# Kernel tuning notes

Hardware: AMD Instinct MI355X
Metric: run time of the kernel (lower is better)

Reference implementation:

```python
import jax, jax.numpy as jnp
import numpy as np

N = 1_000_000
VOCAB = 50_000
EMBED_DIM = 128
ENCODE_DIM = 128


def _random_preorder_tree(n, seed=0):
    """Generate a random tree whose nodes are numbered in pre-order DFS.
    Returns subtree_end[i] = index of the last node in node i's subtree (inclusive)."""
    rng = np.random.default_rng(seed)
    parent = np.empty(n, dtype=np.int64)
    parent[0] = -1
    stack = [0]
    pops = rng.geometric(0.5, size=n) - 1  # how far up to climb before attaching
    for i in range(1, n):
        npop = min(int(pops[i]), len(stack) - 1)
        for _ in range(npop):
            stack.pop()
        parent[i] = stack[-1]
        stack.append(i)
    end = np.arange(n, dtype=np.int64)
    for i in range(n - 1, 0, -1):
        p = parent[i]
        if end[p] < end[i]:
            end[p] = end[i]
    return end


def setup_inputs() -> dict:
    key = jax.random.key(0)
    k1, k2, k3, k4 = jax.random.split(key, 4)
    tokens = jax.random.randint(k1, (N,), 0, VOCAB, dtype=jnp.int64).astype(jnp.int32)
    subtree_end = jnp.asarray(_random_preorder_tree(N), dtype=jnp.int32)
    embedding_weight = jax.random.normal(k2, (VOCAB, EMBED_DIM), dtype=jnp.float32)
    W = jax.random.normal(k3, (ENCODE_DIM, EMBED_DIM), dtype=jnp.float32) * (1.0 / np.sqrt(EMBED_DIM))
    b = jax.random.normal(k4, (ENCODE_DIM,), dtype=jnp.float32) * 0.01
    return {"tokens": tokens, "subtree_end": subtree_end,
            "embedding_weight": embedding_weight, "W": W, "b": b}


def reference(tokens, subtree_end, embedding_weight, W, b):
    # Per-node contribution: x_i = Linear(Embed(token_i))          [N, encode_dim]
    x = embedding_weight[tokens] @ W.T + b
    # h_i = sum of x over subtree(i). With pre-order DFS numbering, the subtree
    # of i is the contiguous range [i, subtree_end[i]], so use an inclusive
    # prefix sum: h_i = S[end_i] - S[i] + x_i.
    S = jnp.cumsum(x, axis=0)                                      # [N, encode_dim]
    h = S[subtree_end] - S + x                                     # [N, encode_dim]
    # pool = max over all node hidden states (order-independent)
    return jnp.max(h, axis=0)                                      # [encode_dim]
```

## Files before the change

kernel.cpp:

```cpp
#include <hip/hip_runtime.h>
#include <hip/hip_bf16.h>

#define D      128
#define LG     8
#define CHUNK  256

typedef __attribute__((ext_vector_type(8))) short          short8;
typedef __attribute__((ext_vector_type(8))) unsigned short ushort8;
typedef __attribute__((ext_vector_type(4))) float          floatx4;

__device__ inline float b2f(unsigned short u) {
    return __uint_as_float(((unsigned)u) << 16);
}
__device__ inline short f2bf(float f) {
    __hip_bfloat16 h = __float2bfloat16(f);
    unsigned short u;
    __builtin_memcpy(&u, &h, 2);
    return (short)u;
}

__global__ void init_out_kernel(float* out, int out_size) {
    int t = threadIdx.x;
    if (t < out_size) out[t] = -INFINITY;
}

__global__ void local_scan_kernel(const int* __restrict__ tokens,
                                  const float* __restrict__ emb,
                                  unsigned short* __restrict__ S,
                                  float* __restrict__ sumE, int n) {
    __shared__ int toks[CHUNK];
    int c  = blockIdx.x;
    int i0 = c << LG;
    int cnt = min(CHUNK, n - i0);
    for (int t = threadIdx.x; t < cnt; t += 128) toks[t] = tokens[i0 + t];
    __syncthreads();
    int d = threadIdx.x;
    float run = 0.f;
    #pragma unroll 8
    for (int j = 0; j < cnt; ++j) {
        run += emb[(size_t)toks[j] * D + d];
        S[(size_t)(i0 + j) * D + d] = (unsigned short)f2bf(run);
    }
    sumE[(size_t)c * D + d] = run;
}

__global__ void scan_kernel(float* sumE, int C) {
    int d    = blockIdx.x;
    int lane = threadIdx.x;
    float carry = 0.f;
    for (int c0 = 0; c0 < C; c0 += 64) {
        int c = c0 + lane;
        float v = (c < C) ? sumE[(size_t)c * D + d] : 0.f;
        float incl = v;
        #pragma unroll
        for (int off = 1; off < 64; off <<= 1) {
            float t = __shfl_up(incl, off);
            if (lane >= off) incl += t;
        }
        if (c < C) sumE[(size_t)c * D + d] = carry + incl - v;
        carry += __shfl(incl, 63);
    }
}

__device__ inline void atomicMaxF(float* addr, float v) {
    if (v >= 0.f) atomicMax((int*)addr, __float_as_int(v));
    else          atomicMin((unsigned int*)addr, __float_as_uint(v));
}

__global__ __launch_bounds__(256, 2) void max_pass_kernel(
        const int* __restrict__ ends, const unsigned short* __restrict__ S,
        const float* __restrict__ prefE, const float* __restrict__ W,
        const float* __restrict__ bvec, float* __restrict__ out, int n) {
    __shared__ ushort8 Sl[257 * 16];
    __shared__ int   s_end[CHUNK];
    __shared__ float red[4][4][16];
    int tid = threadIdx.x;
    int cb  = blockIdx.x;
    int i0  = cb << LG;
    int cnt = min(CHUNK, n - i0);

    for (int t = tid; t < CHUNK; t += 256)
        s_end[t] = (i0 + t < n) ? ends[i0 + t] : (i0 + t);
    const ushort8* gsrc = (const ushort8*)(S + (size_t)i0 * D);
    int units = cnt * 16;
    for (int u = tid; u < units; u += 256) {
        int r = u >> 4, q = u & 15;
        Sl[(r << 4) | (q ^ (r & 7))] = gsrc[u];
    }
    ushort8 z = {0, 0, 0, 0, 0, 0, 0, 0};
    for (int u = units + tid; u < 257 * 16; u += 256) {
        int r = u >> 4, q = u & 15;
        Sl[(r << 4) | (q ^ (r & 7))] = z;
    }

    int lane = tid & 63, wid = tid >> 6;
    int c  = lane & 15;
    int kg = lane >> 4;
    int tw   = wid & 1;
    int pair = wid >> 1;

    short8 Wf[4][4];
    float  bc[4];
    #pragma unroll
    for (int tl = 0; tl < 4; ++tl) {
        int tg = tw * 4 + tl;
        const float* wr = W + (size_t)(tg * 16 + c) * D + kg * 8;
        bc[tl] = bvec[tg * 16 + c];
        #pragma unroll
        for (int kk = 0; kk < 4; ++kk) {
            floatx4 f0 = *(const floatx4*)(wr + kk * 32);
            floatx4 f1 = *(const floatx4*)(wr + kk * 32 + 4);
            short8 w;
            #pragma unroll
            for (int j = 0; j < 4; ++j) { w[j] = f2bf(f0[j]); w[j + 4] = f2bf(f1[j]); }
            Wf[tl][kk] = w;
        }
    }
    float mx[4];
    #pragma unroll
    for (int tl = 0; tl < 4; ++tl) mx[tl] = -INFINITY;

    __syncthreads();

    int tiles = (cnt + 15) >> 4;
    int Tend  = min(pair * 8 + 8, tiles);
    for (int T = pair * 8; T < Tend; ++T) {
        int j    = (T << 4) + c;
        int node = i0 + j;
        bool vr  = node < n;
        int e    = s_end[j];
        int eloc = e - i0;
        bool cross = vr && (eloc >= CHUNK);
        int re = cross ? j : eloc;
        int rp = (j == 0) ? 256 : (j - 1);

        short8 Ae[4], Ap[4];
        #pragma unroll
        for (int kk = 0; kk < 4; ++kk) {
            ushort8 ve = Sl[(re << 4) | ((kk * 4 + kg) ^ (re & 7))];
            ushort8 vp = Sl[(rp << 4) | ((kk * 4 + kg) ^ (rp & 7))];
            __builtin_memcpy(&Ae[kk], &ve, 16);
            __builtin_memcpy(&Ap[kk], &vp, 16);
        }
        if (cross) {
            int ce = e >> LG;
            const ushort8* ge = (const ushort8*)(S + (size_t)e * D);
            const float* qe = prefE + (size_t)ce * D + kg * 8;
            const float* qc = prefE + (size_t)cb * D + kg * 8;
            #pragma unroll
            for (int kk = 0; kk < 4; ++kk) {
                ushort8 se = ge[kk * 4 + kg];
                floatx4 qe0 = *(const floatx4*)(qe + kk * 32);
                floatx4 qe1 = *(const floatx4*)(qe + kk * 32 + 4);
                floatx4 qc0 = *(const floatx4*)(qc + kk * 32);
                floatx4 qc1 = *(const floatx4*)(qc + kk * 32 + 4);
                short8 a;
                #pragma unroll
                for (int jj = 0; jj < 4; ++jj) {
                    a[jj]     = f2bf(b2f(se[jj])     + qe0[jj] - qc0[jj]);
                    a[jj + 4] = f2bf(b2f(se[jj + 4]) + qe1[jj] - qc1[jj]);
                }
                Ae[kk] = a;
            }
        }
        floatx4 cnt4;
        #pragma unroll
        for (int i = 0; i < 4; ++i) {
            int nd = i0 + (T << 4) + kg * 4 + i;
            float ee = (float)__shfl(e, kg * 4 + i);
            cnt4[i] = (nd < n) ? (ee - (float)nd + 1.f) : 0.f;
        }
        #pragma unroll
        for (int tl = 0; tl < 4; ++tl) {
            floatx4 ae = {0.f, 0.f, 0.f, 0.f};
            floatx4 ap = {0.f, 0.f, 0.f, 0.f};
            ae = __builtin_amdgcn_mfma_f32_16x16x32_bf16(Ae[0], Wf[tl][0], ae, 0, 0, 0);
            ae = __builtin_amdgcn_mfma_f32_16x16x32_bf16(Ae[1], Wf[tl][1], ae, 0, 0, 0);
            ae = __builtin_amdgcn_mfma_f32_16x16x32_bf16(Ae[2], Wf[tl][2], ae, 0, 0, 0);
            ae = __builtin_amdgcn_mfma_f32_16x16x32_bf16(Ae[3], Wf[tl][3], ae, 0, 0, 0);
            ap = __builtin_amdgcn_mfma_f32_16x16x32_bf16(Ap[0], Wf[tl][0], ap, 0, 0, 0);
            ap = __builtin_amdgcn_mfma_f32_16x16x32_bf16(Ap[1], Wf[tl][1], ap, 0, 0, 0);
            ap = __builtin_amdgcn_mfma_f32_16x16x32_bf16(Ap[2], Wf[tl][2], ap, 0, 0, 0);
            ap = __builtin_amdgcn_mfma_f32_16x16x32_bf16(Ap[3], Wf[tl][3], ap, 0, 0, 0);
            #pragma unroll
            for (int i = 0; i < 4; ++i) {
                int nd = i0 + (T << 4) + kg * 4 + i;
                float h = (ae[i] - ap[i]) + cnt4[i] * bc[tl];
                if (nd < n) mx[tl] = fmaxf(mx[tl], h);
            }
        }
    }
    #pragma unroll
    for (int tl = 0; tl < 4; ++tl) {
        float v = mx[tl];
        v = fmaxf(v, __shfl_xor(v, 16));
        v = fmaxf(v, __shfl_xor(v, 32));
        mx[tl] = v;
    }
    if (kg == 0) {
        #pragma unroll
        for (int tl = 0; tl < 4; ++tl) red[wid][tl][c] = mx[tl];
    }
    __syncthreads();
    if (tid < 128) {
        int twf = tid >> 6;
        int tl  = (tid >> 4) & 3;
        int cc  = tid & 15;
        float v = fmaxf(red[twf][tl][cc], red[twf + 2][tl][cc]);
        atomicMaxF(&out[(twf * 4 + tl) * 16 + cc], v);
    }
}

extern "C" void kernel_launch(void* const* d_in, const int* in_sizes, int n_in,
                              void* d_out, int out_size, void* d_ws, size_t ws_size,
                              hipStream_t stream) {
    const int*   tokens = (const int*)d_in[0];
    const int*   ends   = (const int*)d_in[1];
    const float* emb    = (const float*)d_in[2];
    const float* W      = (const float*)d_in[3];
    const float* bvec   = (const float*)d_in[4];
    float* out = (float*)d_out;
    int n = in_sizes[0];
    int C = (n + CHUNK - 1) >> LG;

    unsigned short* S    = (unsigned short*)d_ws;
    float*          sumE = (float*)(S + (size_t)n * D);

    init_out_kernel<<<1, 128, 0, stream>>>(out, out_size);
    local_scan_kernel<<<C, 128, 0, stream>>>(tokens, emb, S, sumE, n);
    scan_kernel<<<128, 64, 0, stream>>>(sumE, C);
    max_pass_kernel<<<C, 256, 0, stream>>>(ends, S, sumE, W, bvec, out, n);
}
```

Measured before the change: 331.1 us.

## Fuse projection into local scan and handle in-chunk subtrees before global scan

Applies the linear projection per node with MFMA inside the first kernel, then scans the projected values in shared memory and stores the bf16 chunk-local prefix. In-chunk subtrees are max-reduced in that same kernel, so the second pass only processes nodes whose subtree crosses a chunk boundary, found by ballot. This removes the full re-read of S and the second round of MFMAs over every node. The cost is a serial 256-step shared-memory scan done by only half the threads, and irregular per-node gathers in the cross kernel.

```diff
diff --git a/kernel.cpp b/kernel.cpp
--- a/kernel.cpp
+++ b/kernel.cpp
@@ -8,15 +8,22 @@
 typedef __attribute__((ext_vector_type(8))) short          short8;
 typedef __attribute__((ext_vector_type(8))) unsigned short ushort8;
 typedef __attribute__((ext_vector_type(4))) float          floatx4;
+typedef __attribute__((ext_vector_type(2))) float          floatx2;
+typedef __attribute__((ext_vector_type(2))) unsigned       uintx2;
 
 __device__ inline float b2f(unsigned short u) {
     return __uint_as_float(((unsigned)u) << 16);
 }
-__device__ inline short f2bf(float f) {
+__device__ inline unsigned short f2bf(float f) {
     __hip_bfloat16 h = __float2bfloat16(f);
     unsigned short u;
     __builtin_memcpy(&u, &h, 2);
-    return (short)u;
+    return u;
+}
+
+__device__ inline void atomicMaxF(float* addr, float v) {
+    if (v >= 0.f) atomicMax((int*)addr, __float_as_int(v));
+    else          atomicMin((unsigned int*)addr, __float_as_uint(v));
 }
 
 __global__ void init_out_kernel(float* out, int out_size) {
@@ -24,24 +31,127 @@
     if (t < out_size) out[t] = -INFINITY;
 }
 
-__global__ void local_scan_kernel(const int* __restrict__ tokens,
-                                  const float* __restrict__ emb,
-                                  unsigned short* __restrict__ S,
-                                  float* __restrict__ sumE, int n) {
-    __shared__ int toks[CHUNK];
-    int c  = blockIdx.x;
-    int i0 = c << LG;
-    int cnt = min(CHUNK, n - i0);
-    for (int t = threadIdx.x; t < cnt; t += 128) toks[t] = tokens[i0 + t];
-    __syncthreads();
-    int d = threadIdx.x;
-    float run = 0.f;
-    #pragma unroll 8
-    for (int j = 0; j < cnt; ++j) {
-        run += emb[(size_t)toks[j] * D + d];
-        S[(size_t)(i0 + j) * D + d] = (unsigned short)f2bf(run);
-    }
-    sumE[(size_t)c * D + d] = run;
+__global__ __launch_bounds__(256, 2) void fused_kernel(
+        const int* __restrict__ tokens, const int* __restrict__ ends,
+        const float* __restrict__ emb, const float* __restrict__ W,
+        const float* __restrict__ bvec, unsigned short* __restrict__ T_sp,
+        float* __restrict__ sumE, float* __restrict__ out, int n) {
+    __shared__ ushort8 Tl[CHUNK * 16];
+    __shared__ int s_tok[CHUNK];
+    __shared__ int s_end[CHUNK];
+    __shared__ floatx2 redf[4][64];
+    int tid = threadIdx.x, cb = blockIdx.x;
+    int i0 = cb << LG, cnt = min(CHUNK, n - i0);
+    {
+        int gi = i0 + tid;
+        s_tok[tid] = tokens[min(gi, n - 1)];
+        s_end[tid] = (gi < n) ? ends[gi] : gi;
+    }
+    __syncthreads();
+
+    int lane = tid & 63, wid = tid >> 6;
+    int c = lane & 15, kg = lane >> 4;
+    int tw = wid & 1, pair = wid >> 1;
+
+    short8 Wf[4][4];
+    #pragma unroll
+    for (int tl = 0; tl < 4; ++tl) {
+        const float* wr = W + (size_t)((tw * 4 + tl) * 16 + c) * D + kg * 8;
+        #pragma unroll
+        for (int kk = 0; kk < 4; ++kk) {
+            floatx4 f0 = *(const floatx4*)(wr + kk * 32);
+            floatx4 f1 = *(const floatx4*)(wr + kk * 32 + 4);
+            short8 w;
+            #pragma unroll
+            for (int j = 0; j < 4; ++j) { w[j] = (short)f2bf(f0[j]); w[j + 4] = (short)f2bf(f1[j]); }
+            Wf[tl][kk] = w;
+        }
+    }
+
+    int tiles = (cnt + 15) >> 4;
+    int Tend = min(pair * 8 + 8, tiles);
+    for (int T_ = pair * 8; T_ < Tend; ++T_) {
+        int r = T_ * 16 + c;
+        const float* er = emb + (size_t)s_tok[r] * D + kg * 8;
+        short8 Bf[4];
+        #pragma unroll
+        for (int kk = 0; kk < 4; ++kk) {
+            floatx4 f0 = *(const floatx4*)(er + kk * 32);
+            floatx4 f1 = *(const floatx4*)(er + kk * 32 + 4);
+            short8 bfr;
+            #pragma unroll
+            for (int j = 0; j < 4; ++j) { bfr[j] = (short)f2bf(f0[j]); bfr[j + 4] = (short)f2bf(f1[j]); }
+            Bf[kk] = bfr;
+        }
+        #pragma unroll
+        for (int tl = 0; tl < 4; ++tl) {
+            floatx4 acc = {0.f, 0.f, 0.f, 0.f};
+            acc = __builtin_amdgcn_mfma_f32_16x16x32_bf16(Wf[tl][0], Bf[0], acc, 0, 0, 0);
+            acc = __builtin_amdgcn_mfma_f32_16x16x32_bf16(Wf[tl][1], Bf[1], acc, 0, 0, 0);
+            acc = __builtin_amdgcn_mfma_f32_16x16x32_bf16(Wf[tl][2], Bf[2], acc, 0, 0, 0);
+            acc = __builtin_amdgcn_mfma_f32_16x16x32_bf16(Wf[tl][3], Bf[3], acc, 0, 0, 0);
+            int to = tw * 4 + tl;
+            int gs = (to * 2 + (kg >> 1)) ^ (r & 7);
+            unsigned u0 = ((unsigned)f2bf(acc[0])) | (((unsigned)f2bf(acc[1])) << 16);
+            unsigned u1 = ((unsigned)f2bf(acc[2])) | (((unsigned)f2bf(acc[3])) << 16);
+            uintx2 uu = {u0, u1};
+            *(uintx2*)((char*)Tl + r * 256 + gs * 16 + (kg & 1) * 8) = uu;
+        }
+    }
+    __syncthreads();
+
+    if (tid < 128) {
+        int d = tid, gr = d >> 3, o = d & 7;
+        unsigned short* Tb = (unsigned short*)Tl;
+        float acc = 0.f;
+        for (int j = 0; j < cnt; ++j) {
+            int idx = j * 128 + (((gr ^ (j & 7))) << 3) + o;
+            acc += b2f(Tb[idx]);
+            Tb[idx] = f2bf(acc);
+        }
+        sumE[(size_t)cb * D + d] = acc;
+    }
+    __syncthreads();
+
+    {
+        int units = cnt * 16;
+        ushort8* go = (ushort8*)(T_sp + (size_t)i0 * D);
+        for (int u = tid; u < units; u += 256) {
+            int r = u >> 4, q = u & 15;
+            go[u] = Tl[(r << 4) | (q ^ (r & 7))];
+        }
+    }
+
+    floatx2 bl = *(const floatx2*)(bvec + lane * 2);
+    floatx2 hm = {-INFINITY, -INFINITY};
+    for (int rr = 0; rr < 64; ++rr) {
+        int j = wid * 64 + rr;
+        if (j >= cnt) break;
+        int e = s_end[j];
+        int eloc = e - i0;
+        if (eloc >= CHUNK) continue;
+        int gre = (lane >> 2) ^ (eloc & 7);
+        unsigned se = *(const unsigned*)((const char*)Tl + eloc * 256 + (gre << 4) + (lane & 3) * 4);
+        unsigned sp = 0u;
+        if (j > 0) {
+            int grp = (lane >> 2) ^ ((j - 1) & 7);
+            sp = *(const unsigned*)((const char*)Tl + (j - 1) * 256 + (grp << 4) + (lane & 3) * 4);
+        }
+        float cf = (float)(e - (i0 + j) + 1);
+        float h0 = b2f((unsigned short)(se & 0xffff)) - b2f((unsigned short)(sp & 0xffff)) + cf * bl[0];
+        float h1 = b2f((unsigned short)(se >> 16))    - b2f((unsigned short)(sp >> 16))    + cf * bl[1];
+        hm[0] = fmaxf(hm[0], h0);
+        hm[1] = fmaxf(hm[1], h1);
+    }
+    redf[wid][lane] = hm;
+    __syncthreads();
+    if (tid < 64) {
+        floatx2 a = redf[0][tid], b = redf[1][tid], cc = redf[2][tid], dd = redf[3][tid];
+        float v0 = fmaxf(fmaxf(a[0], b[0]), fmaxf(cc[0], dd[0]));
+        float v1 = fmaxf(fmaxf(a[1], b[1]), fmaxf(cc[1], dd[1]));
+        atomicMaxF(&out[tid * 2],     v0);
+        atomicMaxF(&out[tid * 2 + 1], v1);
+    }
 }
 
 __global__ void scan_kernel(float* sumE, int C) {
@@ -62,152 +172,50 @@
     }
 }
 
-__device__ inline void atomicMaxF(float* addr, float v) {
-    if (v >= 0.f) atomicMax((int*)addr, __float_as_int(v));
-    else          atomicMin((unsigned int*)addr, __float_as_uint(v));
-}
-
-__global__ __launch_bounds__(256, 2) void max_pass_kernel(
-        const int* __restrict__ ends, const unsigned short* __restrict__ S,
-        const float* __restrict__ prefE, const float* __restrict__ W,
-        const float* __restrict__ bvec, float* __restrict__ out, int n) {
-    __shared__ ushort8 Sl[257 * 16];
-    __shared__ int   s_end[CHUNK];
-    __shared__ float red[4][4][16];
-    int tid = threadIdx.x;
-    int cb  = blockIdx.x;
-    int i0  = cb << LG;
-    int cnt = min(CHUNK, n - i0);
-
-    for (int t = tid; t < CHUNK; t += 256)
-        s_end[t] = (i0 + t < n) ? ends[i0 + t] : (i0 + t);
-    const ushort8* gsrc = (const ushort8*)(S + (size_t)i0 * D);
-    int units = cnt * 16;
-    for (int u = tid; u < units; u += 256) {
-        int r = u >> 4, q = u & 15;
-        Sl[(r << 4) | (q ^ (r & 7))] = gsrc[u];
-    }
-    ushort8 z = {0, 0, 0, 0, 0, 0, 0, 0};
-    for (int u = units + tid; u < 257 * 16; u += 256) {
-        int r = u >> 4, q = u & 15;
-        Sl[(r << 4) | (q ^ (r & 7))] = z;
-    }
-
-    int lane = tid & 63, wid = tid >> 6;
-    int c  = lane & 15;
-    int kg = lane >> 4;
-    int tw   = wid & 1;
-    int pair = wid >> 1;
-
-    short8 Wf[4][4];
-    float  bc[4];
-    #pragma unroll
-    for (int tl = 0; tl < 4; ++tl) {
-        int tg = tw * 4 + tl;
-        const float* wr = W + (size_t)(tg * 16 + c) * D + kg * 8;
-        bc[tl] = bvec[tg * 16 + c];
-        #pragma unroll
-        for (int kk = 0; kk < 4; ++kk) {
-            floatx4 f0 = *(const floatx4*)(wr + kk * 32);
-            floatx4 f1 = *(const floatx4*)(wr + kk * 32 + 4);
-            short8 w;
-            #pragma unroll
-            for (int j = 0; j < 4; ++j) { w[j] = f2bf(f0[j]); w[j + 4] = f2bf(f1[j]); }
-            Wf[tl][kk] = w;
-        }
-    }
-    float mx[4];
-    #pragma unroll
-    for (int tl = 0; tl < 4; ++tl) mx[tl] = -INFINITY;
-
-    __syncthreads();
-
-    int tiles = (cnt + 15) >> 4;
-    int Tend  = min(pair * 8 + 8, tiles);
-    for (int T = pair * 8; T < Tend; ++T) {
-        int j    = (T << 4) + c;
-        int node = i0 + j;
-        bool vr  = node < n;
-        int e    = s_end[j];
-        int eloc = e - i0;
-        bool cross = vr && (eloc >= CHUNK);
-        int re = cross ? j : eloc;
-        int rp = (j == 0) ? 256 : (j - 1);
-
-        short8 Ae[4], Ap[4];
-        #pragma unroll
-        for (int kk = 0; kk < 4; ++kk) {
-            ushort8 ve = Sl[(re << 4) | ((kk * 4 + kg) ^ (re & 7))];
-            ushort8 vp = Sl[(rp << 4) | ((kk * 4 + kg) ^ (rp & 7))];
-            __builtin_memcpy(&Ae[kk], &ve, 16);
-            __builtin_memcpy(&Ap[kk], &vp, 16);
-        }
-        if (cross) {
-            int ce = e >> LG;
-            const ushort8* ge = (const ushort8*)(S + (size_t)e * D);
-            const float* qe = prefE + (size_t)ce * D + kg * 8;
-            const float* qc = prefE + (size_t)cb * D + kg * 8;
-            #pragma unroll
-            for (int kk = 0; kk < 4; ++kk) {
-                ushort8 se = ge[kk * 4 + kg];
-                floatx4 qe0 = *(const floatx4*)(qe + kk * 32);
-                floatx4 qe1 = *(const floatx4*)(qe + kk * 32 + 4);
-                floatx4 qc0 = *(const floatx4*)(qc + kk * 32);
-                floatx4 qc1 = *(const floatx4*)(qc + kk * 32 + 4);
-                short8 a;
-                #pragma unroll
-                for (int jj = 0; jj < 4; ++jj) {
-                    a[jj]     = f2bf(b2f(se[jj])     + qe0[jj] - qc0[jj]);
-                    a[jj + 4] = f2bf(b2f(se[jj + 4]) + qe1[jj] - qc1[jj]);
-                }
-                Ae[kk] = a;
-            }
-        }
-        floatx4 cnt4;
-        #pragma unroll
-        for (int i = 0; i < 4; ++i) {
-            int nd = i0 + (T << 4) + kg * 4 + i;
-            float ee = (float)__shfl(e, kg * 4 + i);
-            cnt4[i] = (nd < n) ? (ee - (float)nd + 1.f) : 0.f;
-        }
-        #pragma unroll
-        for (int tl = 0; tl < 4; ++tl) {
-            floatx4 ae = {0.f, 0.f, 0.f, 0.f};
-            floatx4 ap = {0.f, 0.f, 0.f, 0.f};
-            ae = __builtin_amdgcn_mfma_f32_16x16x32_bf16(Ae[0], Wf[tl][0], ae, 0, 0, 0);
-            ae = __builtin_amdgcn_mfma_f32_16x16x32_bf16(Ae[1], Wf[tl][1], ae, 0, 0, 0);
-            ae = __builtin_amdgcn_mfma_f32_16x16x32_bf16(Ae[2], Wf[tl][2], ae, 0, 0, 0);
-            ae = __builtin_amdgcn_mfma_f32_16x16x32_bf16(Ae[3], Wf[tl][3], ae, 0, 0, 0);
-            ap = __builtin_amdgcn_mfma_f32_16x16x32_bf16(Ap[0], Wf[tl][0], ap, 0, 0, 0);
-            ap = __builtin_amdgcn_mfma_f32_16x16x32_bf16(Ap[1], Wf[tl][1], ap, 0, 0, 0);
-            ap = __builtin_amdgcn_mfma_f32_16x16x32_bf16(Ap[2], Wf[tl][2], ap, 0, 0, 0);
-            ap = __builtin_amdgcn_mfma_f32_16x16x32_bf16(Ap[3], Wf[tl][3], ap, 0, 0, 0);
-            #pragma unroll
-            for (int i = 0; i < 4; ++i) {
-                int nd = i0 + (T << 4) + kg * 4 + i;
-                float h = (ae[i] - ap[i]) + cnt4[i] * bc[tl];
-                if (nd < n) mx[tl] = fmaxf(mx[tl], h);
-            }
-        }
-    }
-    #pragma unroll
-    for (int tl = 0; tl < 4; ++tl) {
-        float v = mx[tl];
-        v = fmaxf(v, __shfl_xor(v, 16));
-        v = fmaxf(v, __shfl_xor(v, 32));
-        mx[tl] = v;
-    }
-    if (kg == 0) {
-        #pragma unroll
-        for (int tl = 0; tl < 4; ++tl) red[wid][tl][c] = mx[tl];
-    }
-    __syncthreads();
-    if (tid < 128) {
-        int twf = tid >> 6;
-        int tl  = (tid >> 4) & 3;
-        int cc  = tid & 15;
-        float v = fmaxf(red[twf][tl][cc], red[twf + 2][tl][cc]);
-        atomicMaxF(&out[(twf * 4 + tl) * 16 + cc], v);
+__global__ __launch_bounds__(256, 4) void cross_kernel(
+        const int* __restrict__ ends, const unsigned short* __restrict__ T_sp,
+        const float* __restrict__ pref, const float* __restrict__ bvec,
+        float* __restrict__ out, int n) {
+    __shared__ floatx2 redf[4][64];
+    int tid = threadIdx.x, lane = tid & 63, wid = tid >> 6;
+    floatx2 bl = *(const floatx2*)(bvec + lane * 2);
+    floatx2 hm = {-INFINITY, -INFINITY};
+    int nw = (n + 63) >> 6;
+    int gw = blockIdx.x * 4 + wid, stride = gridDim.x * 4;
+    for (int w = gw; w < nw; w += stride) {
+        int i = w * 64 + lane;
+        int e = (i < n) ? ends[i] : 0;
+        bool cross = (i < n) && ((e >> LG) != (i >> LG));
+        unsigned long long mask = __ballot(cross);
+        while (mask) {
+            int b = __builtin_ctzll(mask);
+            mask &= mask - 1;
+            int ii = w * 64 + b;
+            int ee = __shfl(e, b);
+            int ci = ii >> LG, ce = ee >> LG;
+            unsigned se = *(const unsigned*)(T_sp + (size_t)ee * D + lane * 2);
+            unsigned sp = 0u;
+            if (ii & (CHUNK - 1))
+                sp = *(const unsigned*)(T_sp + (size_t)(ii - 1) * D + lane * 2);
+            floatx2 pe = *(const floatx2*)(pref + (size_t)ce * D + lane * 2);
+            floatx2 pc = *(const floatx2*)(pref + (size_t)ci * D + lane * 2);
+            float cf = (float)(ee - ii + 1);
+            float h0 = (b2f((unsigned short)(se & 0xffff)) + pe[0])
+                     - (b2f((unsigned short)(sp & 0xffff)) + pc[0]) + cf * bl[0];
+            float h1 = (b2f((unsigned short)(se >> 16)) + pe[1])
+                     - (b2f((unsigned short)(sp >> 16)) + pc[1]) + cf * bl[1];
+            hm[0] = fmaxf(hm[0], h0);
+            hm[1] = fmaxf(hm[1], h1);
+        }
+    }
+    redf[wid][lane] = hm;
+    __syncthreads();
+    if (tid < 64) {
+        floatx2 a = redf[0][tid], b = redf[1][tid], cc = redf[2][tid], dd = redf[3][tid];
+        float v0 = fmaxf(fmaxf(a[0], b[0]), fmaxf(cc[0], dd[0]));
+        float v1 = fmaxf(fmaxf(a[1], b[1]), fmaxf(cc[1], dd[1]));
+        atomicMaxF(&out[tid * 2],     v0);
+        atomicMaxF(&out[tid * 2 + 1], v1);
     }
 }
 
@@ -223,11 +231,12 @@
     int n = in_sizes[0];
     int C = (n + CHUNK - 1) >> LG;
 
-    unsigned short* S    = (unsigned short*)d_ws;
-    float*          sumE = (float*)(S + (size_t)n * D);
+    unsigned short* T_sp = (unsigned short*)d_ws;
+    float*          sumE = (float*)(T_sp + (size_t)n * D);
 
     init_out_kernel<<<1, 128, 0, stream>>>(out, out_size);
-    local_scan_kernel<<<C, 128, 0, stream>>>(tokens, emb, S, sumE, n);
+    fused_kernel<<<C, 256, 0, stream>>>(tokens, ends, emb, W, bvec,
+                                        T_sp, sumE, out, n);
     scan_kernel<<<128, 64, 0, stream>>>(sumE, C);
-    max_pass_kernel<<<C, 256, 0, stream>>>(ends, S, sumE, W, bvec, out, n);
-}
+    cross_kernel<<<512, 256, 0, stream>>>(ends, T_sp, sumE, bvec, out, n);
+}
```

Result: slower. 465.1 us (+40.5%).
